# Kernel optimization log

Hardware: AMD Instinct MI355X
Metric: run time of the kernel (lower is better)

Reference implementation:

```python
import jax, jax.numpy as jnp
import numpy as np

B, T, E, H = 2, 2048, 1024, 16
Dh = E // H  # head_size = 64


def setup_inputs() -> dict:
    key = jax.random.key(0)
    ks = jax.random.split(key, 6)
    s = E ** -0.5
    x = jax.random.normal(ks[0], (B, T, E), dtype=jnp.float32)
    Wq = jax.random.normal(ks[1], (H, E, Dh), dtype=jnp.float32) * s
    Wk = jax.random.normal(ks[2], (H, E, Dh), dtype=jnp.float32) * s
    Wv = jax.random.normal(ks[3], (H, E, Dh), dtype=jnp.float32) * s
    wo_w = jax.random.normal(ks[4], (E, E), dtype=jnp.float32) * s  # torch Linear weight [out,in]
    wo_b = jax.random.normal(ks[5], (E,), dtype=jnp.float32) * 0.01
    return {"x": x, "Wq": Wq, "Wk": Wk, "Wv": Wv, "wo_w": wo_w, "wo_b": wo_b}


def reference(x, Wq, Wk, Wv, wo_w, wo_b):
    # Batched equivalent of the per-head Python loop: project all heads at once.
    q = jnp.einsum('bte,hed->bhtd', x, Wq)
    k = jnp.einsum('bte,hed->bhtd', x, Wk)
    v = jnp.einsum('bte,hed->bhtd', x, Wv)
    scale = Dh ** -0.5
    scores = jnp.einsum('bhtd,bhsd->bhts', q, k) * scale  # [B,H,T,T]
    causal = jnp.tril(jnp.ones((T, T), dtype=bool))
    scores = jnp.where(causal, scores, jnp.finfo(scores.dtype).min)
    att = jax.nn.softmax(scores, axis=-1)
    out = jnp.einsum('bhts,bhsd->bhtd', att, v)  # [B,H,T,Dh]
    # concat heads (head order along last dim, matching torch.cat over heads)
    out = out.transpose(0, 2, 1, 3).reshape(B, T, E)
    return out @ wo_w.T + wo_b
```

## Files before the change

### kernel.cpp

```cpp
#include <hip/hip_runtime.h>

#define B_ 2
#define T_ 2048
#define E_ 1024
#define H_ 16
#define DH 64

typedef unsigned short u16;
typedef unsigned int u32;
typedef __bf16 bf16x8 __attribute__((ext_vector_type(8)));
typedef float f32x4 __attribute__((ext_vector_type(4)));

__device__ __forceinline__ u16 f2bf(float f) {
  u32 u = __builtin_bit_cast(u32, f);
  u = u + 0x7FFFu + ((u >> 16) & 1u);
  return (u16)(u >> 16);
}
__device__ __forceinline__ float bf2f(u16 v) {
  return __builtin_bit_cast(float, (u32)v << 16);
}
__device__ __forceinline__ bf16x8 ldfrag(const u16* p) { return *(const bf16x8*)p; }

__device__ __forceinline__ void gload_lds16(const u16* g, u16* l) {
  __builtin_amdgcn_global_load_lds((const __attribute__((address_space(1))) u32*)g,
                                   (__attribute__((address_space(3))) u32*)l, 16, 0, 0);
}

__global__ __launch_bounds__(256) void k_conv_all(const float* __restrict__ x,
                                                  const float* __restrict__ Wq,
                                                  const float* __restrict__ Wk,
                                                  const float* __restrict__ Wv,
                                                  const float* __restrict__ wo_w,
                                                  u16* __restrict__ xb, u16* __restrict__ wT,
                                                  u16* __restrict__ woB) {
  __shared__ __align__(16) u16 Ls[64][68];
  const int t = threadIdx.x;
  const int bx = blockIdx.x;
  if (bx < 2048 || bx >= 2816) {
    const float* src = (bx < 2048) ? x : wo_w;
    u16* dst = (bx < 2048) ? xb : woB;
    u32 i = (((bx < 2048) ? bx : (bx - 2816)) * 256u + t) * 8u;
    float4 a = *(const float4*)(src + i);
    float4 b = *(const float4*)(src + i + 4);
    uint4 v;
    v.x = (u32)f2bf(a.x) | ((u32)f2bf(a.y) << 16);
    v.y = (u32)f2bf(a.z) | ((u32)f2bf(a.w) << 16);
    v.z = (u32)f2bf(b.x) | ((u32)f2bf(b.y) << 16);
    v.w = (u32)f2bf(b.z) | ((u32)f2bf(b.w) << 16);
    *(uint4*)(dst + i) = v;
    return;
  }
  const int idx = bx - 2048;
  const int e0 = (idx & 15) * 64;
  const int h = (idx >> 4) & 15;
  const int which = idx >> 8;
  const float* src = (which == 0) ? Wq : ((which == 1) ? Wk : Wv);
  const float scale = (which == 0) ? 0.18033688011112042f : 1.0f;
#pragma unroll
  for (int p = 0; p < 4; p++) {
    int id2 = p * 256 + t;
    int row = id2 >> 4, ch = id2 & 15;
    float4 v = *(const float4*)(src + ((size_t)h * E_ + e0 + row) * DH + ch * 4);
    uint2 pk;
    pk.x = (u32)f2bf(v.x * scale) | ((u32)f2bf(v.y * scale) << 16);
    pk.y = (u32)f2bf(v.z * scale) | ((u32)f2bf(v.w * scale) << 16);
    *(uint2*)(&Ls[row][ch * 4]) = pk;
  }
  __syncthreads();
  u16* dst = wT + ((size_t)which * H_ + h) * (DH * E_);
#pragma unroll
  for (int p = 0; p < 4; p++) {
    int id2 = p * 256 + t;
    int d = id2 >> 4, ec = id2 & 15;
    uint2 pk;
    pk.x = (u32)Ls[ec * 4 + 0][d] | ((u32)Ls[ec * 4 + 1][d] << 16);
    pk.y = (u32)Ls[ec * 4 + 2][d] | ((u32)Ls[ec * 4 + 3][d] << 16);
    *(uint2*)(dst + (size_t)d * E_ + e0 + ec * 4) = pk;
  }
}

__global__ __launch_bounds__(256, 3) void k_qkv(const u16* __restrict__ xb, const u16* __restrict__ wT,
                                                u16* __restrict__ Qb, u16* __restrict__ Kb,
                                                u16* __restrict__ VbT) {
  __shared__ __align__(16) u16 As[128 * 64];
  __shared__ __align__(16) u16 Bs[128 * 64];
  const int tid = threadIdx.x;
  const int w = tid >> 6, lane = tid & 63, quad = lane >> 4, lr = lane & 15;
  const int wr = w >> 1, wc = w & 1;
  const int t0 = blockIdx.x * 128;
  const int n0 = blockIdx.y * 128;
  const int sr = lane >> 3, sc = lane & 7;

  f32x4 acc[4][4];
  const f32x4 z4 = {0.f, 0.f, 0.f, 0.f};
#pragma unroll
  for (int i = 0; i < 4; i++)
#pragma unroll
    for (int j = 0; j < 4; j++) acc[i][j] = z4;

  for (int k0 = 0; k0 < E_; k0 += 64) {
    __syncthreads();
#pragma unroll
    for (int ii = 0; ii < 4; ii++) {
      int ra = w * 32 + ii * 8 + sr;
      gload_lds16(xb + (size_t)(t0 + ra) * E_ + k0 + ((sc ^ (ra & 7)) << 3),
                  As + (w * 32 + ii * 8) * 64);
      gload_lds16(wT + (size_t)(n0 + ra) * E_ + k0 + ((sc ^ (ra & 7)) << 3),
                  Bs + (w * 32 + ii * 8) * 64);
    }
    __syncthreads();
#pragma unroll
    for (int kk = 0; kk < 2; kk++) {
      bf16x8 af[4], bfv[4];
#pragma unroll
      for (int rt = 0; rt < 4; rt++) {
        int row = wr * 64 + rt * 16 + lr;
        af[rt] = ldfrag(As + row * 64 + (((kk * 4 + quad) ^ (row & 7)) << 3));
      }
#pragma unroll
      for (int ct = 0; ct < 4; ct++) {
        int row = wc * 64 + ct * 16 + lr;
        bfv[ct] = ldfrag(Bs + row * 64 + (((kk * 4 + quad) ^ (row & 7)) << 3));
      }
#pragma unroll
      for (int rt = 0; rt < 4; rt++)
#pragma unroll
        for (int ct = 0; ct < 4; ct++)
          acc[rt][ct] = __builtin_amdgcn_mfma_f32_16x16x32_bf16(af[rt], bfv[ct], acc[rt][ct], 0, 0, 0);
    }
  }

  const int qkv = n0 >> 10;
  if (qkv < 2) {
    u16* outp = (qkv == 0) ? Qb : Kb;
#pragma unroll
    for (int rt = 0; rt < 4; rt++)
#pragma unroll
      for (int ct = 0; ct < 4; ct++) {
        int n = n0 + wc * 64 + ct * 16 + lr;
        int h = (n >> 6) & 15, d = n & 63;
#pragma unroll
        for (int r = 0; r < 4; r++) {
          int t = t0 + wr * 64 + rt * 16 + quad * 4 + r;
          int bb = t >> 11, tt = t & 2047;
          outp[(((size_t)bb * H_ + h) * T_ + tt) * DH + d] = f2bf(acc[rt][ct][r]);
        }
      }
  } else {
#pragma unroll
    for (int rt = 0; rt < 4; rt++)
#pragma unroll
      for (int ct = 0; ct < 4; ct++) {
        int n = n0 + wc * 64 + ct * 16 + lr;
        int h = (n >> 6) & 15, d = n & 63;
        int t = t0 + wr * 64 + rt * 16 + quad * 4;
        int bb = t >> 11, tt = t & 2047;
        uint2 pk;
        pk.x = (u32)f2bf(acc[rt][ct][0]) | ((u32)f2bf(acc[rt][ct][1]) << 16);
        pk.y = (u32)f2bf(acc[rt][ct][2]) | ((u32)f2bf(acc[rt][ct][3]) << 16);
        *(uint2*)(VbT + (((size_t)bb * H_ + h) * DH + d) * T_ + tt) = pk;
      }
  }
}

__global__ __launch_bounds__(256, 4) void k_attn(const u16* __restrict__ Qb, const u16* __restrict__ Kb,
                                                 const u16* __restrict__ VbT, u16* __restrict__ O0,
                                                 u16* __restrict__ O1, float* __restrict__ Lb) {
  __shared__ __align__(16) u16 KV[2][8192];
  __shared__ __align__(16) u16 Ps[4096];
  const int tid = threadIdx.x;
  const int w = tid >> 6, lane = tid & 63, quad = lane >> 4, lr = lane & 15;
  const int l7 = lr & 7;
  const int srow = lane >> 3, schunk = lane & 7;
  const int i = blockIdx.x >> 1, s = blockIdx.x & 1;
  const int h = blockIdx.y, bb = blockIdx.z;
  const u16* qb = Qb + ((size_t)bb * H_ + h) * (size_t)(T_ * DH);
  const u16* kb = Kb + ((size_t)bb * H_ + h) * (size_t)(T_ * DH);
  const u16* vbT = VbT + ((size_t)bb * H_ + h) * (size_t)(T_ * DH);
  const f32x4 z4 = {0.f, 0.f, 0.f, 0.f};
  const float MFIX = 20.0f;

  for (int jb = 0; jb < 2; jb++) {
    const int qt = jb ? i : (31 - i);
    const int sg = jb ? (1 - s) : s;
    const int t0 = qt * 64;
    __syncthreads();

    const u16* qrow = qb + (size_t)(t0 + w * 16 + lr) * DH;
    bf16x8 bq0 = ldfrag(qrow + quad * 8);
    bf16x8 bq1 = ldfrag(qrow + 32 + quad * 8);

    f32x4 o_acc[4];
#pragma unroll
    for (int dt = 0; dt < 4; dt++) o_acc[dt] = z4;
    float l_i = 0.f;

    int cur = 0;
    if (sg <= qt) {
      int j0 = sg * 64;
#pragma unroll
      for (int ii = 0; ii < 2; ii++) {
        int r = w * 16 + ii * 8 + srow;
        gload_lds16(kb + (size_t)(j0 + r) * DH + ((schunk ^ (r & 7)) << 3),
                    KV[0] + (w * 16 + ii * 8) * 64);
        gload_lds16(vbT + (size_t)r * T_ + j0 + ((schunk ^ (r & 7)) << 3),
                    KV[0] + 4096 + (w * 16 + ii * 8) * 64);
      }
    }

    for (int jt = sg; jt <= qt; jt += 2) {
      __syncthreads();
      if (jt + 2 <= qt) {
        int j0n = (jt + 2) * 64;
#pragma unroll
        for (int ii = 0; ii < 2; ii++) {
          int r = w * 16 + ii * 8 + srow;
          gload_lds16(kb + (size_t)(j0n + r) * DH + ((schunk ^ (r & 7)) << 3),
                      KV[cur ^ 1] + (w * 16 + ii * 8) * 64);
          gload_lds16(vbT + (size_t)r * T_ + j0n + ((schunk ^ (r & 7)) << 3),
                      KV[cur ^ 1] + 4096 + (w * 16 + ii * 8) * 64);
        }
      }
      const u16* Ks = KV[cur];
      const u16* Vts = KV[cur] + 4096;

      f32x4 s_acc[4];
#pragma unroll
      for (int st = 0; st < 4; st++) s_acc[st] = z4;
#pragma unroll
      for (int st = 0; st < 4; st++) {
        bf16x8 ak0 = ldfrag(Ks + (st * 16 + lr) * 64 + ((quad ^ l7) << 3));
        bf16x8 ak1 = ldfrag(Ks + (st * 16 + lr) * 64 + (((4 + quad) ^ l7) << 3));
        s_acc[st] = __builtin_amdgcn_mfma_f32_16x16x32_bf16(ak0, bq0, s_acc[st], 0, 0, 0);
        s_acc[st] = __builtin_amdgcn_mfma_f32_16x16x32_bf16(ak1, bq1, s_acc[st], 0, 0, 0);
      }

      if (jt == qt) {
        int qloc = w * 16 + lr;
#pragma unroll
        for (int st = 0; st < 4; st++) {
          int sbase = st * 16 + quad * 4;
#pragma unroll
          for (int r = 0; r < 4; r++)
            if (sbase + r > qloc) s_acc[st][r] = -__builtin_inff();
        }
      }

      float rsum = 0.f;
#pragma unroll
      for (int st = 0; st < 4; st++) {
        float p0 = __builtin_amdgcn_exp2f(s_acc[st][0] - MFIX);
        float p1 = __builtin_amdgcn_exp2f(s_acc[st][1] - MFIX);
        float p2 = __builtin_amdgcn_exp2f(s_acc[st][2] - MFIX);
        float p3 = __builtin_amdgcn_exp2f(s_acc[st][3] - MFIX);
        rsum += (p0 + p1) + (p2 + p3);
        uint2 pk;
        pk.x = (__builtin_bit_cast(u32, p0) >> 16) | (__builtin_bit_cast(u32, p1) & 0xffff0000u);
        pk.y = (__builtin_bit_cast(u32, p2) >> 16) | (__builtin_bit_cast(u32, p3) & 0xffff0000u);
        *(uint2*)(Ps + (w * 16 + lr) * 64 + (((st * 2 + (quad >> 1)) ^ l7) << 3) + ((quad & 1) << 2)) = pk;
      }
      l_i += rsum;

#pragma unroll
      for (int kk = 0; kk < 2; kk++) {
        bf16x8 bp = ldfrag(Ps + (w * 16 + lr) * 64 + (((kk * 4 + quad) ^ l7) << 3));
#pragma unroll
        for (int dt = 0; dt < 4; dt++) {
          bf16x8 av = ldfrag(Vts + (dt * 16 + lr) * 64 + (((kk * 4 + quad) ^ l7) << 3));
          o_acc[dt] = __builtin_amdgcn_mfma_f32_16x16x32_bf16(av, bp, o_acc[dt], 0, 0, 0);
        }
      }
      cur ^= 1;
    }

    l_i += __shfl_xor(l_i, 16);
    l_i += __shfl_xor(l_i, 32);

    u16* op = (sg == 0) ? O0 : O1;
    int t = t0 + w * 16 + lr;
    u16* orow = op + ((size_t)bb * T_ + t) * E_ + h * DH;
#pragma unroll
    for (int dt = 0; dt < 4; dt++) {
      uint2 pk;
      pk.x = (u32)f2bf(o_acc[dt][0]) | ((u32)f2bf(o_acc[dt][1]) << 16);
      pk.y = (u32)f2bf(o_acc[dt][2]) | ((u32)f2bf(o_acc[dt][3]) << 16);
      *(uint2*)(orow + dt * 16 + quad * 4) = pk;
    }
    if (quad == 0) {
      Lb[((sg * B_ + bb) * H_ + h) * T_ + t] = l_i;
    }
  }
}

__global__ __launch_bounds__(256, 2) void k_oproj(const u16* __restrict__ O0, const u16* __restrict__ O1,
                                                  const float* __restrict__ Lb, const u16* __restrict__ woB,
                                                  const float* __restrict__ bias, float* __restrict__ out) {
  __shared__ __align__(16) u16 As[64 * 64];
  __shared__ __align__(16) u16 Bs[128 * 64];
  const int tid = threadIdx.x;
  const int w = tid >> 6, lane = tid & 63, quad = lane >> 4, lr = lane & 15;
  const int r0 = blockIdx.x * 64, n0 = blockIdx.y * 128;
  const int sr = lane >> 3, sc = lane & 7;
  const int arow = tid >> 2, acseg = (tid & 3) * 16;
  const int agr = r0 + arow;
  const int abb = agr >> 11, att = agr & 2047;

  f32x4 acc[4][2];
  const f32x4 z4 = {0.f, 0.f, 0.f, 0.f};
#pragma unroll
  for (int i = 0; i < 4; i++)
#pragma unroll
    for (int j = 0; j < 2; j++) acc[i][j] = z4;

  for (int k0 = 0; k0 < E_; k0 += 64) {
    const int hh = k0 >> 6;
    __syncthreads();
    {
      int lidx = ((0 * B_ + abb) * H_ + hh) * T_ + att;
      float l0 = Lb[lidx], l1 = Lb[lidx + B_ * H_ * T_];
      float a = 1.0f / (l0 + l1);
      const u16* p0 = O0 + (size_t)agr * E_ + k0 + acseg;
      const u16* p1 = O1 + (size_t)agr * E_ + k0 + acseg;
      uint4 u0a = *(const uint4*)p0, u0b = *(const uint4*)(p0 + 8);
      uint4 u1a = *(const uint4*)p1, u1b = *(const uint4*)(p1 + 8);
      uint4 m0, m1;
      u32 t0, t1;
#define MRG(ua, ub) (t0 = (u32)f2bf((bf2f((u16)(ua)) + bf2f((u16)(ub))) * a),                  \
                     t1 = (u32)f2bf((bf2f((u16)((ua) >> 16)) + bf2f((u16)((ub) >> 16))) * a),  \
                     t0 | (t1 << 16))
      m0.x = MRG(u0a.x, u1a.x); m0.y = MRG(u0a.y, u1a.y);
      m0.z = MRG(u0a.z, u1a.z); m0.w = MRG(u0a.w, u1a.w);
      m1.x = MRG(u0b.x, u1b.x); m1.y = MRG(u0b.y, u1b.y);
      m1.z = MRG(u0b.z, u1b.z); m1.w = MRG(u0b.w, u1b.w);
#undef MRG
      int c0 = (tid & 3) * 2;
      *(uint4*)(As + arow * 64 + ((c0 ^ (arow & 7)) << 3)) = m0;
      *(uint4*)(As + arow * 64 + (((c0 + 1) ^ (arow & 7)) << 3)) = m1;
    }
#pragma unroll
    for (int ii = 0; ii < 4; ii++) {
      int rb = w * 32 + ii * 8 + sr;
      gload_lds16(woB + (size_t)(n0 + rb) * E_ + k0 + ((sc ^ (rb & 7)) << 3),
                  Bs + (w * 32 + ii * 8) * 64);
    }
    __syncthreads();
#pragma unroll
    for (int kk = 0; kk < 2; kk++) {
      bf16x8 af[4], bfv[2];
#pragma unroll
      for (int rt = 0; rt < 4; rt++) {
        int row = rt * 16 + lr;
        af[rt] = ldfrag(As + row * 64 + (((kk * 4 + quad) ^ (row & 7)) << 3));
      }
#pragma unroll
      for (int ct = 0; ct < 2; ct++) {
        int row = w * 32 + ct * 16 + lr;
        bfv[ct] = ldfrag(Bs + row * 64 + (((kk * 4 + quad) ^ (row & 7)) << 3));
      }
#pragma unroll
      for (int rt = 0; rt < 4; rt++)
#pragma unroll
        for (int ct = 0; ct < 2; ct++)
          acc[rt][ct] = __builtin_amdgcn_mfma_f32_16x16x32_bf16(af[rt], bfv[ct], acc[rt][ct], 0, 0, 0);
    }
  }

#pragma unroll
  for (int ct = 0; ct < 2; ct++) {
    int col = n0 + w * 32 + ct * 16 + lr;
    float bv = bias[col];
#pragma unroll
    for (int rt = 0; rt < 4; rt++)
#pragma unroll
      for (int r = 0; r < 4; r++) {
        int row = r0 + rt * 16 + quad * 4 + r;
        out[(size_t)row * E_ + col] = acc[rt][ct][r] + bv;
      }
  }
}

extern "C" void kernel_launch(void* const* d_in, const int* in_sizes, int n_in,
                              void* d_out, int out_size, void* d_ws, size_t ws_size,
                              hipStream_t stream) {
  const float* x = (const float*)d_in[0];
  const float* Wq = (const float*)d_in[1];
  const float* Wk = (const float*)d_in[2];
  const float* Wv = (const float*)d_in[3];
  const float* wo_w = (const float*)d_in[4];
  const float* wo_b = (const float*)d_in[5];
  float* out = (float*)d_out;
  char* ws = (char*)d_ws;

  u16* xb  = (u16*)(ws + 0);
  u16* wT  = (u16*)(ws + 8388608);
  u16* woB = (u16*)(ws + 14680064);
  u16* Qb  = (u16*)(ws + 16777216);
  u16* Kb  = (u16*)(ws + 25165824);
  u16* VbT = (u16*)(ws + 33554432);
  u16* O0  = (u16*)(ws + 41943040);
  u16* O1  = xb;
  float* Lb = (float*)(ws + 8388608);

  k_conv_all<<<3328, 256, 0, stream>>>(x, Wq, Wk, Wv, wo_w, xb, wT, woB);
  k_qkv<<<dim3(32, 24), 256, 0, stream>>>(xb, wT, Qb, Kb, VbT);
  k_attn<<<dim3(32, 16, 2), 256, 0, stream>>>(Qb, Kb, VbT, O0, O1, Lb);
  k_oproj<<<dim3(64, 8), 256, 0, stream>>>(O0, O1, Lb, woB, wo_b, out);
}
```

Measured before the change: 174.9 us.

## Split attention KV range three ways and add separate combine kernel

```diff
diff --git a/kernel.cpp b/kernel.cpp
--- a/kernel.cpp
+++ b/kernel.cpp
@@ -163,28 +163,29 @@
   }
 }
 
-__global__ __launch_bounds__(256, 4) void k_attn(const u16* __restrict__ Qb, const u16* __restrict__ Kb,
+__global__ __launch_bounds__(256, 6) void k_attn(const u16* __restrict__ Qb, const u16* __restrict__ Kb,
                                                  const u16* __restrict__ VbT, u16* __restrict__ O0,
-                                                 u16* __restrict__ O1, float* __restrict__ Lb) {
-  __shared__ __align__(16) u16 KV[2][8192];
+                                                 u16* __restrict__ O1, u16* __restrict__ O2,
+                                                 float* __restrict__ Lb) {
+  __shared__ __align__(16) u16 Ks[4096];
+  __shared__ __align__(16) u16 Vts[4096];
   __shared__ __align__(16) u16 Ps[4096];
   const int tid = threadIdx.x;
   const int w = tid >> 6, lane = tid & 63, quad = lane >> 4, lr = lane & 15;
   const int l7 = lr & 7;
   const int srow = lane >> 3, schunk = lane & 7;
-  const int i = blockIdx.x >> 1, s = blockIdx.x & 1;
+  const int i = blockIdx.x / 3, s = blockIdx.x - 3 * i;
   const int h = blockIdx.y, bb = blockIdx.z;
   const u16* qb = Qb + ((size_t)bb * H_ + h) * (size_t)(T_ * DH);
   const u16* kb = Kb + ((size_t)bb * H_ + h) * (size_t)(T_ * DH);
   const u16* vbT = VbT + ((size_t)bb * H_ + h) * (size_t)(T_ * DH);
   const f32x4 z4 = {0.f, 0.f, 0.f, 0.f};
   const float MFIX = 20.0f;
+  u16* const ops[3] = {O0, O1, O2};
 
   for (int jb = 0; jb < 2; jb++) {
     const int qt = jb ? i : (31 - i);
-    const int sg = jb ? (1 - s) : s;
     const int t0 = qt * 64;
-    __syncthreads();
 
     const u16* qrow = qb + (size_t)(t0 + w * 16 + lr) * DH;
     bf16x8 bq0 = ldfrag(qrow + quad * 8);
@@ -195,34 +196,18 @@
     for (int dt = 0; dt < 4; dt++) o_acc[dt] = z4;
     float l_i = 0.f;
 
-    int cur = 0;
-    if (sg <= qt) {
-      int j0 = sg * 64;
+    for (int jt = s; jt <= qt; jt += 3) {
+      const int j0 = jt * 64;
+      __syncthreads();
 #pragma unroll
       for (int ii = 0; ii < 2; ii++) {
         int r = w * 16 + ii * 8 + srow;
         gload_lds16(kb + (size_t)(j0 + r) * DH + ((schunk ^ (r & 7)) << 3),
-                    KV[0] + (w * 16 + ii * 8) * 64);
+                    Ks + (w * 16 + ii * 8) * 64);
         gload_lds16(vbT + (size_t)r * T_ + j0 + ((schunk ^ (r & 7)) << 3),
-                    KV[0] + 4096 + (w * 16 + ii * 8) * 64);
-      }
-    }
-
-    for (int jt = sg; jt <= qt; jt += 2) {
+                    Vts + (w * 16 + ii * 8) * 64);
+      }
       __syncthreads();
-      if (jt + 2 <= qt) {
-        int j0n = (jt + 2) * 64;
-#pragma unroll
-        for (int ii = 0; ii < 2; ii++) {
-          int r = w * 16 + ii * 8 + srow;
-          gload_lds16(kb + (size_t)(j0n + r) * DH + ((schunk ^ (r & 7)) << 3),
-                      KV[cur ^ 1] + (w * 16 + ii * 8) * 64);
-          gload_lds16(vbT + (size_t)r * T_ + j0n + ((schunk ^ (r & 7)) << 3),
-                      KV[cur ^ 1] + 4096 + (w * 16 + ii * 8) * 64);
-        }
-      }
-      const u16* Ks = KV[cur];
-      const u16* Vts = KV[cur] + 4096;
 
       f32x4 s_acc[4];
 #pragma unroll
@@ -270,13 +255,12 @@
           o_acc[dt] = __builtin_amdgcn_mfma_f32_16x16x32_bf16(av, bp, o_acc[dt], 0, 0, 0);
         }
       }
-      cur ^= 1;
     }
 
     l_i += __shfl_xor(l_i, 16);
     l_i += __shfl_xor(l_i, 32);
 
-    u16* op = (sg == 0) ? O0 : O1;
+    u16* op = ops[s];
     int t = t0 + w * 16 + lr;
     u16* orow = op + ((size_t)bb * T_ + t) * E_ + h * DH;
 #pragma unroll
@@ -287,13 +271,38 @@
       *(uint2*)(orow + dt * 16 + quad * 4) = pk;
     }
     if (quad == 0) {
-      Lb[((sg * B_ + bb) * H_ + h) * T_ + t] = l_i;
-    }
-  }
-}
-
-__global__ __launch_bounds__(256, 2) void k_oproj(const u16* __restrict__ O0, const u16* __restrict__ O1,
-                                                  const float* __restrict__ Lb, const u16* __restrict__ woB,
+      Lb[((s * B_ + bb) * H_ + h) * T_ + t] = l_i;
+    }
+  }
+}
+
+__global__ void k_combine(const u16* __restrict__ O0, const u16* __restrict__ O1,
+                          const u16* __restrict__ O2, const float* __restrict__ Lb,
+                          u16* __restrict__ AO) {
+  int idx = blockIdx.x * 256 + threadIdx.x;
+  int e0 = idx * 8;
+  int bb = e0 >> 21, t = (e0 >> 10) & 2047, hh = (e0 >> 6) & 15;
+  const int S = B_ * H_ * T_;
+  int r = (bb * H_ + hh) * T_ + t;
+  float a = 1.0f / (Lb[r] + Lb[r + S] + Lb[r + 2 * S]);
+  uint4 u0 = *(const uint4*)(O0 + e0);
+  uint4 u1 = *(const uint4*)(O1 + e0);
+  uint4 u2 = *(const uint4*)(O2 + e0);
+  uint4 o;
+  u32 lo, hi;
+#define MRG3(a0, a1, a2) (lo = (u32)f2bf((bf2f((u16)(a0)) + bf2f((u16)(a1)) + bf2f((u16)(a2))) * a),  \
+                          hi = (u32)f2bf((bf2f((u16)((a0) >> 16)) + bf2f((u16)((a1) >> 16)) +          \
+                                          bf2f((u16)((a2) >> 16))) * a),                               \
+                          lo | (hi << 16))
+  o.x = MRG3(u0.x, u1.x, u2.x);
+  o.y = MRG3(u0.y, u1.y, u2.y);
+  o.z = MRG3(u0.z, u1.z, u2.z);
+  o.w = MRG3(u0.w, u1.w, u2.w);
+#undef MRG3
+  *(uint4*)(AO + e0) = o;
+}
+
+__global__ __launch_bounds__(256, 4) void k_oproj(const u16* __restrict__ AO, const u16* __restrict__ woB,
                                                   const float* __restrict__ bias, float* __restrict__ out) {
   __shared__ __align__(16) u16 As[64 * 64];
   __shared__ __align__(16) u16 Bs[128 * 64];
@@ -301,9 +310,6 @@
   const int w = tid >> 6, lane = tid & 63, quad = lane >> 4, lr = lane & 15;
   const int r0 = blockIdx.x * 64, n0 = blockIdx.y * 128;
   const int sr = lane >> 3, sc = lane & 7;
-  const int arow = tid >> 2, acseg = (tid & 3) * 16;
-  const int agr = r0 + arow;
-  const int abb = agr >> 11, att = agr & 2047;
 
   f32x4 acc[4][2];
   const f32x4 z4 = {0.f, 0.f, 0.f, 0.f};
@@ -313,29 +319,12 @@
     for (int j = 0; j < 2; j++) acc[i][j] = z4;
 
   for (int k0 = 0; k0 < E_; k0 += 64) {
-    const int hh = k0 >> 6;
     __syncthreads();
-    {
-      int lidx = ((0 * B_ + abb) * H_ + hh) * T_ + att;
-      float l0 = Lb[lidx], l1 = Lb[lidx + B_ * H_ * T_];
-      float a = 1.0f / (l0 + l1);
-      const u16* p0 = O0 + (size_t)agr * E_ + k0 + acseg;
-      const u16* p1 = O1 + (size_t)agr * E_ + k0 + acseg;
-      uint4 u0a = *(const uint4*)p0, u0b = *(const uint4*)(p0 + 8);
-      uint4 u1a = *(const uint4*)p1, u1b = *(const uint4*)(p1 + 8);
-      uint4 m0, m1;
-      u32 t0, t1;
-#define MRG(ua, ub) (t0 = (u32)f2bf((bf2f((u16)(ua)) + bf2f((u16)(ub))) * a),                  \
-                     t1 = (u32)f2bf((bf2f((u16)((ua) >> 16)) + bf2f((u16)((ub) >> 16))) * a),  \
-                     t0 | (t1 << 16))
-      m0.x = MRG(u0a.x, u1a.x); m0.y = MRG(u0a.y, u1a.y);
-      m0.z = MRG(u0a.z, u1a.z); m0.w = MRG(u0a.w, u1a.w);
-      m1.x = MRG(u0b.x, u1b.x); m1.y = MRG(u0b.y, u1b.y);
-      m1.z = MRG(u0b.z, u1b.z); m1.w = MRG(u0b.w, u1b.w);
-#undef MRG
-      int c0 = (tid & 3) * 2;
-      *(uint4*)(As + arow * 64 + ((c0 ^ (arow & 7)) << 3)) = m0;
-      *(uint4*)(As + arow * 64 + (((c0 + 1) ^ (arow & 7)) << 3)) = m1;
+#pragma unroll
+    for (int ii = 0; ii < 2; ii++) {
+      int ra = w * 16 + ii * 8 + sr;
+      gload_lds16(AO + (size_t)(r0 + ra) * E_ + k0 + ((sc ^ (ra & 7)) << 3),
+                  As + (w * 16 + ii * 8) * 64);
     }
 #pragma unroll
     for (int ii = 0; ii < 4; ii++) {
@@ -399,10 +388,13 @@
   u16* VbT = (u16*)(ws + 33554432);
   u16* O0  = (u16*)(ws + 41943040);
   u16* O1  = xb;
+  u16* O2  = (u16*)(ws + 50331648);
+  u16* AO  = (u16*)(ws + 58720256);
   float* Lb = (float*)(ws + 8388608);
 
   k_conv_all<<<3328, 256, 0, stream>>>(x, Wq, Wk, Wv, wo_w, xb, wT, woB);
   k_qkv<<<dim3(32, 24), 256, 0, stream>>>(xb, wT, Qb, Kb, VbT);
-  k_attn<<<dim3(32, 16, 2), 256, 0, stream>>>(Qb, Kb, VbT, O0, O1, Lb);
-  k_oproj<<<dim3(64, 8), 256, 0, stream>>>(O0, O1, Lb, woB, wo_b, out);
-}
+  k_attn<<<dim3(96, 16, 2), 256, 0, stream>>>(Qb, Kb, VbT, O0, O1, O2, Lb);
+  k_combine<<<2048, 256, 0, stream>>>(O0, O1, O2, Lb, AO);
+  k_oproj<<<dim3(64, 8), 256, 0, stream>>>(AO, woB, wo_b, out);
+}
```

Result: slower. 213.2 us (+21.9%).
